# Kernel optimization log

Hardware: AMD Instinct MI355X
Metric: run time of the kernel (lower is better)

## Reference

```python
import jax, jax.numpy as jnp
import numpy as np

B = 1024          # batch
H = W = 64        # image height/width
WIN = 2           # patch window (non-overlapping 2x2)
N = (H // WIN) * (W // WIN)   # 1024 DNPU nodes
N_ELEC = 7        # electrodes per DNPU device
N_IN = 4
N_CTRL = 3        # control electrodes per node
HID = 90          # surrogate MLP hidden width
OUT = 32          # out_size (OUT*OUT == N)


def setup_inputs() -> dict:
    key = jax.random.key(0)
    ks = jax.random.split(key, 8)
    x = jax.random.normal(ks[0], (B, 1, H, W), jnp.float32)
    # learned control voltages per node, in a typical DNPU voltage range
    controls = jax.random.uniform(ks[1], (N, N_CTRL), jnp.float32, -1.2, 0.6)
    # per-node electrode assignment: random permutation of the 7 electrodes;
    # first 4 are data-input electrodes, last 3 are control electrodes
    perms = jax.vmap(lambda k: jax.random.permutation(k, N_ELEC))(
        jax.random.split(ks[2], N))
    inputs_list = perms[:, :N_IN].astype(jnp.int32)
    control_list = perms[:, N_IN:].astype(jnp.int32)
    # shared surrogate-model MLP (7 -> 90 -> 90 -> 1)
    W1 = jax.random.normal(ks[3], (N_ELEC, HID), jnp.float32) * 0.3
    b1 = jax.random.normal(ks[4], (HID,), jnp.float32) * 0.1
    W2 = jax.random.normal(ks[5], (HID, HID), jnp.float32) * 0.1
    b2 = jax.random.normal(ks[6], (HID,), jnp.float32) * 0.1
    W3 = jax.random.normal(ks[7], (HID, 1), jnp.float32) * 0.1
    b3 = jnp.zeros((1,), jnp.float32)
    return {"x": x, "controls": controls, "W1": W1, "b1": b1,
            "W2": W2, "b2": b2, "W3": W3, "b3": b3,
            "inputs_list": inputs_list, "control_list": control_list}


def reference(x, controls, W1, b1, W2, b2, W3, b3, inputs_list, control_list):
    Bx = x.shape[0]
    # nf.unfold(x, kernel_size=2, stride=2): element order (c, kh, kw),
    # blocks row-major over spatial positions -> [B, 4, N]
    p = x.reshape(Bx, 1, H // WIN, WIN, W // WIN, WIN)
    p = p.transpose(0, 1, 3, 5, 2, 4).reshape(Bx, WIN * WIN, N)
    patches = p.transpose(0, 2, 1)                       # [B, N, 4]
    # assemble the 7-electrode input per node (vectorized scatter over nodes)
    node = jnp.arange(N)[:, None]
    E = jnp.zeros((Bx, N, N_ELEC), x.dtype)
    E = E.at[:, node, inputs_list].set(patches)          # data electrodes
    E = E.at[:, node, control_list].set(
        jnp.broadcast_to(controls, (Bx, N, N_CTRL)))     # control electrodes
    # shared surrogate MLP applied to every (batch, node) electrode vector
    h = jax.nn.elu(jnp.einsum('bne,eh->bnh', E, W1) + b1)  # [B, N, 90]
    h = jax.nn.elu(h @ W2 + b2)                            # [B, N, 90]
    out = (h @ W3 + b3)[..., 0]                            # [B, N] (concat over nodes)
    return out.reshape(-1, OUT, OUT)                       # out_size view
```

## Files before the change

### kernel.cpp

```cpp
#include <hip/hip_runtime.h>
#include <stdint.h>


#define HID 90

typedef float  f32x4 __attribute__((ext_vector_type(4)));
typedef _Float16 f16x8 __attribute__((ext_vector_type(8)));

#define WS_W1P 0
#define WS_B2V 720
#define WS_W3V 816
#define WS_B3  912
#define WS_W2F 928
#define WS_TOT_ELEMS (928 + 9216)

__global__ void prep_kernel(const float* __restrict__ W1, const float* __restrict__ b1,
                            const float* __restrict__ W2, const float* __restrict__ b2,
                            const float* __restrict__ W3, const float* __restrict__ b3,
                            float* __restrict__ wsf)
{
    _Float16* w2f = (_Float16*)(wsf + WS_W2F);
    for (int i = blockIdx.x * blockDim.x + threadIdx.x; i < WS_TOT_ELEMS;
         i += gridDim.x * blockDim.x) {
        if (i < 928) {
            float v = 0.f;
            if (i < WS_B2V) {
                const int k = i >> 3, e = i & 7;
                v = (e < 7) ? W1[e * HID + k] : b1[k];
            } else if (i < WS_W3V) {
                const int j = i - WS_B2V; v = (j < HID) ? b2[j] : 0.f;
            } else if (i < WS_B3) {
                const int j = i - WS_W3V; v = (j < HID) ? W3[j] : 0.f;
            } else if (i == WS_B3) {
                v = b3[0];
            }
            wsf[i] = v;
        } else {
            const int e  = i - 928;
            const int f  = e >> 9;
            const int r  = e & 511;
            const int l  = r >> 3, ii = r & 7;
            const int ks = f / 6, jt = f - ks * 6;
            const int k  = ks * 32 + ((l >> 4) << 3) + ii;
            const int j  = jt * 16 + (l & 15);
            const float v = (k < HID && j < HID) ? W2[k * HID + j] : 0.f;
            w2f[e] = (_Float16)v;
        }
    }
}

__device__ __forceinline__ float elu_f(float x) {
    return fmaxf(x, 0.f) + (__expf(fminf(x, 0.f)) - 1.f);
}

__device__ __forceinline__ uint32_t pk_f16(float a, float b) {
    auto r = __builtin_amdgcn_cvt_pkrtz(a, b);
    return __builtin_bit_cast(uint32_t, r);
}

__global__ __launch_bounds__(256, 3)
void dnpu_main(const float* __restrict__ x,
               const float* __restrict__ controls,
               const int* __restrict__ inputs_list,
               const int* __restrict__ control_list,
               const float* __restrict__ wsf,
               float* __restrict__ out)
{
    __shared__ alignas(16) _Float16 Hs[4 * 3 * 4 * 64 * 8];

    const int t    = threadIdx.x;
    const int row  = blockIdx.x * 256 + t;
    const int b    = row >> 10;
    const int n    = row & 1023;
    const int ph   = n >> 5, pw = n & 31;
    const int w    = t >> 6;
    const int lane = t & 63;
    const int rt_w = lane >> 4;
    const int lj   = lane & 15;

    const float* xp = x + ((size_t)b << 12) + (ph * 2) * 64 + pw * 2;
    const float2 pA = *(const float2*)xp;
    const float2 pB = *(const float2*)(xp + 64);

    const int4 il  = *(const int4*)(inputs_list + (n << 2));
    const int  cl0 = control_list[n * 3 + 0];
    const int  cl1 = control_list[n * 3 + 1];
    const int  cl2 = control_list[n * 3 + 2];
    const float c0 = controls[n * 3 + 0];
    const float c1 = controls[n * 3 + 1];
    const float c2 = controls[n * 3 + 2];

    float E[8];
    E[7] = 1.0f;
#pragma unroll
    for (int e = 0; e < 7; ++e) {
        float v = 0.f;
        v = (il.x == e) ? pA.x : v;
        v = (il.y == e) ? pA.y : v;
        v = (il.z == e) ? pB.x : v;
        v = (il.w == e) ? pB.y : v;
        v = (cl0 == e) ? c0 : v;
        v = (cl1 == e) ? c1 : v;
        v = (cl2 == e) ? c2 : v;
        E[e] = v;
    }

    const float* W1P = wsf + WS_W1P;
#pragma unroll
    for (int ks = 0; ks < 3; ++ks) {
#pragma unroll
        for (int lg = 0; lg < 4; ++lg) {
            uint32_t pk4[4];
#pragma unroll
            for (int p = 0; p < 4; ++p) {
                const int k = ks * 32 + lg * 8 + p * 2;
                if (k < HID) {
                    const float* wA = W1P + (k << 3);
                    float pa0 = 0.f, pa1 = 0.f, pb0 = 0.f, pb1 = 0.f;
#pragma unroll
                    for (int e = 0; e < 8; e += 2) {
                        pa0 = __builtin_fmaf(E[e],     wA[e],     pa0);
                        pa1 = __builtin_fmaf(E[e + 1], wA[e + 1], pa1);
                        pb0 = __builtin_fmaf(E[e],     wA[e + 8], pb0);
                        pb1 = __builtin_fmaf(E[e + 1], wA[e + 9], pb1);
                    }
                    pk4[p] = pk_f16(elu_f(pa0 + pa1), elu_f(pb0 + pb1));
                } else {
                    pk4[p] = 0u;
                }
            }
            const int slot = ((w * 3 + ks) * 4 + rt_w) * 64 + lg * 16 + lj;
            uint4 v4; v4.x = pk4[0]; v4.y = pk4[1]; v4.z = pk4[2]; v4.w = pk4[3];
            *(uint4*)&Hs[slot * 8] = v4;
        }
    }

    const float* B2V = wsf + WS_B2V;
    const float* W3V = wsf + WS_W3V;
    float b2j[6], w3j[6];
#pragma unroll
    for (int jt = 0; jt < 6; ++jt) {
        b2j[jt] = B2V[jt * 16 + lj];
        w3j[jt] = W3V[jt * 16 + lj];
    }
    const float B3v = wsf[WS_B3];

    const _Float16* w2f = (const _Float16*)(wsf + WS_W2F);
    f32x4 psum[4];
#pragma unroll
    for (int rt = 0; rt < 4; ++rt) psum[rt] = (f32x4){0.f, 0.f, 0.f, 0.f};

#pragma unroll
    for (int jt = 0; jt < 6; ++jt) {
        f32x4 acc[4];
#pragma unroll
        for (int rt = 0; rt < 4; ++rt)
            acc[rt] = (f32x4){b2j[jt], b2j[jt], b2j[jt], b2j[jt]};
#pragma unroll
        for (int ks = 0; ks < 3; ++ks) {
            const f16x8 bfr = *(const f16x8*)(w2f + (((ks * 6 + jt) * 64 + lane) << 3));
#pragma unroll
            for (int rt = 0; rt < 4; ++rt) {
                const f16x8 afr = *(const f16x8*)&Hs[(((w * 3 + ks) * 4 + rt) * 64 + lane) * 8];
                acc[rt] = __builtin_amdgcn_mfma_f32_16x16x32_f16(afr, bfr, acc[rt], 0, 0, 0);
            }
        }
        const float w3 = w3j[jt];
#pragma unroll
        for (int rt = 0; rt < 4; ++rt) {
            psum[rt][0] = __builtin_fmaf(elu_f(acc[rt][0]), w3, psum[rt][0]);
            psum[rt][1] = __builtin_fmaf(elu_f(acc[rt][1]), w3, psum[rt][1]);
            psum[rt][2] = __builtin_fmaf(elu_f(acc[rt][2]), w3, psum[rt][2]);
            psum[rt][3] = __builtin_fmaf(elu_f(acc[rt][3]), w3, psum[rt][3]);
        }
    }

    const int lg = lane >> 4;
    const int rowbase = blockIdx.x * 256 + w * 64;
#pragma unroll
    for (int rt = 0; rt < 4; ++rt) {
        float p0 = psum[rt][0], p1 = psum[rt][1], p2 = psum[rt][2], p3 = psum[rt][3];
#pragma unroll
        for (int mask = 1; mask < 16; mask <<= 1) {
            p0 += __shfl_xor(p0, mask);
            p1 += __shfl_xor(p1, mask);
            p2 += __shfl_xor(p2, mask);
            p3 += __shfl_xor(p3, mask);
        }
        if (lj < 4) {
            const float v = (lj == 0) ? p0 : (lj == 1) ? p1 : (lj == 2) ? p2 : p3;
            out[rowbase + rt * 16 + 4 * lg + lj] = v + B3v;
        }
    }
}

extern "C" void kernel_launch(void* const* d_in, const int* in_sizes, int n_in,
                              void* d_out, int out_size, void* d_ws, size_t ws_size,
                              hipStream_t stream)
{
    const float* x          = (const float*)d_in[0];
    const float* controls   = (const float*)d_in[1];
    const float* W1         = (const float*)d_in[2];
    const float* b1         = (const float*)d_in[3];
    const float* W2         = (const float*)d_in[4];
    const float* b2         = (const float*)d_in[5];
    const float* W3         = (const float*)d_in[6];
    const float* b3         = (const float*)d_in[7];
    const int* inputs_list  = (const int*)d_in[8];
    const int* control_list = (const int*)d_in[9];
    float* out = (float*)d_out;
    float* wsf = (float*)d_ws;

    hipLaunchKernelGGL(prep_kernel, dim3(40), dim3(256), 0, stream,
                       W1, b1, W2, b2, W3, b3, wsf);
    hipLaunchKernelGGL(dnpu_main, dim3(4096), dim3(256), 0, stream,
                       x, controls, inputs_list, control_list, wsf, out);
}
```

Measured before the change: 153.5 us.

## Compute first MLP layer with MFMA instead of scalar FMAs

After: 137.6 us. -10.3%, faster.

```diff
diff --git a/kernel.cpp b/kernel.cpp
--- a/kernel.cpp
+++ b/kernel.cpp
@@ -7,12 +7,17 @@
 typedef float  f32x4 __attribute__((ext_vector_type(4)));
 typedef _Float16 f16x8 __attribute__((ext_vector_type(8)));
 
-#define WS_W1P 0
-#define WS_B2V 720
-#define WS_W3V 816
-#define WS_B3  912
-#define WS_W2F 928
-#define WS_TOT_ELEMS (928 + 9216)
+#define WS_W1A 0
+#define WS_B2V 1536
+#define WS_W3V 1632
+#define WS_B3  1728
+#define WS_W2F 1744
+#define WS_TOT_ITEMS (1744 + 9216)
+
+__device__ __forceinline__ uint32_t pk_f16(float a, float b) {
+    auto r = __builtin_amdgcn_cvt_pkrtz(a, b);
+    return __builtin_bit_cast(uint32_t, r);
+}
 
 __global__ void prep_kernel(const float* __restrict__ W1, const float* __restrict__ b1,
                             const float* __restrict__ W2, const float* __restrict__ b2,
@@ -20,23 +25,29 @@
                             float* __restrict__ wsf)
 {
     _Float16* w2f = (_Float16*)(wsf + WS_W2F);
-    for (int i = blockIdx.x * blockDim.x + threadIdx.x; i < WS_TOT_ELEMS;
+    for (int i = blockIdx.x * blockDim.x + threadIdx.x; i < WS_TOT_ITEMS;
          i += gridDim.x * blockDim.x) {
-        if (i < 928) {
+        if (i < WS_B2V) {
+            const int mt = i >> 8;
+            const int l  = (i >> 2) & 63;
+            const int dp = i & 3;
+            const int hi = l >> 4, lj = l & 15;
+            const int m  = mt * 16 + lj;
+            float v0 = 0.f, v1 = 0.f;
+            if (hi == 0 && m < HID) {
+                const int e0 = 2 * dp, e1 = 2 * dp + 1;
+                v0 = (e0 < 7) ? W1[e0 * HID + m] : b1[m];
+                v1 = (e1 < 7) ? W1[e1 * HID + m] : b1[m];
+            }
+            wsf[i] = __builtin_bit_cast(float, pk_f16(v0, v1));
+        } else if (i < WS_W2F) {
             float v = 0.f;
-            if (i < WS_B2V) {
-                const int k = i >> 3, e = i & 7;
-                v = (e < 7) ? W1[e * HID + k] : b1[k];
-            } else if (i < WS_W3V) {
-                const int j = i - WS_B2V; v = (j < HID) ? b2[j] : 0.f;
-            } else if (i < WS_B3) {
-                const int j = i - WS_W3V; v = (j < HID) ? W3[j] : 0.f;
-            } else if (i == WS_B3) {
-                v = b3[0];
-            }
+            if (i < WS_W3V)      { const int j = i - WS_B2V; v = (j < HID) ? b2[j] : 0.f; }
+            else if (i < WS_B3)  { const int j = i - WS_W3V; v = (j < HID) ? W3[j] : 0.f; }
+            else if (i == WS_B3) { v = b3[0]; }
             wsf[i] = v;
         } else {
-            const int e  = i - 928;
+            const int e  = i - WS_W2F;
             const int f  = e >> 9;
             const int r  = e & 511;
             const int l  = r >> 3, ii = r & 7;
@@ -51,11 +62,6 @@
 
 __device__ __forceinline__ float elu_f(float x) {
     return fmaxf(x, 0.f) + (__expf(fminf(x, 0.f)) - 1.f);
-}
-
-__device__ __forceinline__ uint32_t pk_f16(float a, float b) {
-    auto r = __builtin_amdgcn_cvt_pkrtz(a, b);
-    return __builtin_bit_cast(uint32_t, r);
 }
 
 __global__ __launch_bounds__(256, 3)
@@ -75,8 +81,9 @@
     const int ph   = n >> 5, pw = n & 31;
     const int w    = t >> 6;
     const int lane = t & 63;
-    const int rt_w = lane >> 4;
+    const int hi   = lane >> 4;
     const int lj   = lane & 15;
+    const bool hi0 = (hi == 0);
 
     const float* xp = x + ((size_t)b << 12) + (ph * 2) * 64 + pw * 2;
     const float2 pA = *(const float2*)xp;
@@ -90,8 +97,7 @@
     const float c1 = controls[n * 3 + 1];
     const float c2 = controls[n * 3 + 2];
 
-    float E[8];
-    E[7] = 1.0f;
+    float E[7];
 #pragma unroll
     for (int e = 0; e < 7; ++e) {
         float v = 0.f;
@@ -104,34 +110,45 @@
         v = (cl2 == e) ? c2 : v;
         E[e] = v;
     }
-
-    const float* W1P = wsf + WS_W1P;
-#pragma unroll
-    for (int ks = 0; ks < 3; ++ks) {
-#pragma unroll
-        for (int lg = 0; lg < 4; ++lg) {
-            uint32_t pk4[4];
-#pragma unroll
-            for (int p = 0; p < 4; ++p) {
-                const int k = ks * 32 + lg * 8 + p * 2;
-                if (k < HID) {
-                    const float* wA = W1P + (k << 3);
-                    float pa0 = 0.f, pa1 = 0.f, pb0 = 0.f, pb1 = 0.f;
-#pragma unroll
-                    for (int e = 0; e < 8; e += 2) {
-                        pa0 = __builtin_fmaf(E[e],     wA[e],     pa0);
-                        pa1 = __builtin_fmaf(E[e + 1], wA[e + 1], pa1);
-                        pb0 = __builtin_fmaf(E[e],     wA[e + 8], pb0);
-                        pb1 = __builtin_fmaf(E[e + 1], wA[e + 9], pb1);
-                    }
-                    pk4[p] = pk_f16(elu_f(pa0 + pa1), elu_f(pb0 + pb1));
-                } else {
-                    pk4[p] = 0u;
-                }
-            }
-            const int slot = ((w * 3 + ks) * 4 + rt_w) * 64 + lg * 16 + lj;
-            uint4 v4; v4.x = pk4[0]; v4.y = pk4[1]; v4.z = pk4[2]; v4.w = pk4[3];
-            *(uint4*)&Hs[slot * 8] = v4;
+    const uint32_t ep0 = pk_f16(E[0], E[1]);
+    const uint32_t ep1 = pk_f16(E[2], E[3]);
+    const uint32_t ep2 = pk_f16(E[4], E[5]);
+    const uint32_t ep3 = pk_f16(E[6], 1.0f);
+
+    uint4 bfe[4];
+#pragma unroll
+    for (int ct = 0; ct < 4; ++ct) {
+        const int src = ct * 16 + lj;
+        const uint32_t s0 = (uint32_t)__shfl((int)ep0, src);
+        const uint32_t s1 = (uint32_t)__shfl((int)ep1, src);
+        const uint32_t s2 = (uint32_t)__shfl((int)ep2, src);
+        const uint32_t s3 = (uint32_t)__shfl((int)ep3, src);
+        bfe[ct].x = hi0 ? s0 : 0u;
+        bfe[ct].y = hi0 ? s1 : 0u;
+        bfe[ct].z = hi0 ? s2 : 0u;
+        bfe[ct].w = hi0 ? s3 : 0u;
+    }
+
+    const uint32_t* w1a = (const uint32_t*)(wsf + WS_W1A);
+    const int k0    = 4 * hi;
+#pragma unroll
+    for (int mt = 0; mt < 6; ++mt) {
+        const uint4 au = *(const uint4*)(w1a + mt * 256 + lane * 4);
+        const f16x8 afr = __builtin_bit_cast(f16x8, au);
+        const int kk   = mt * 16 + k0;
+        const int ks   = kk >> 5;
+        const int hi2  = (kk & 31) >> 3;
+        const int dpair = (kk & 7) >> 1;
+#pragma unroll
+        for (int ct = 0; ct < 4; ++ct) {
+            f32x4 c = (f32x4){0.f, 0.f, 0.f, 0.f};
+            c = __builtin_amdgcn_mfma_f32_16x16x32_f16(
+                afr, __builtin_bit_cast(f16x8, bfe[ct]), c, 0, 0, 0);
+            const uint32_t d0 = pk_f16(elu_f(c[0]), elu_f(c[1]));
+            const uint32_t d1 = pk_f16(elu_f(c[2]), elu_f(c[3]));
+            const int slot = ((w * 3 + ks) * 4 + ct) * 64 + hi2 * 16 + lj;
+            uint2 v2; v2.x = d0; v2.y = d1;
+            *(uint2*)&Hs[slot * 8 + dpair * 2] = v2;
         }
     }
 
@@ -175,7 +192,6 @@
         }
     }
 
-    const int lg = lane >> 4;
     const int rowbase = blockIdx.x * 256 + w * 64;
 #pragma unroll
     for (int rt = 0; rt < 4; ++rt) {
@@ -189,7 +205,7 @@
         }
         if (lj < 4) {
             const float v = (lj == 0) ? p0 : (lj == 1) ? p1 : (lj == 2) ? p2 : p3;
-            out[rowbase + rt * 16 + 4 * lg + lj] = v + B3v;
+            out[rowbase + rt * 16 + 4 * hi + lj] = v + B3v;
         }
     }
 }
@@ -211,7 +227,7 @@
     float* out = (float*)d_out;
     float* wsf = (float*)d_ws;
 
-    hipLaunchKernelGGL(prep_kernel, dim3(40), dim3(256), 0, stream,
+    hipLaunchKernelGGL(prep_kernel, dim3(48), dim3(256), 0, stream,
                        W1, b1, W2, b2, W3, b3, wsf);
     hipLaunchKernelGGL(dnpu_main, dim3(4096), dim3(256), 0, stream,
                        x, controls, inputs_list, control_list, wsf, out);
```
